# Kernel optimization log

Hardware: AMD Instinct MI355X
Metric: run time of the kernel (lower is better)

The kernel has to match this reference:

```python
import jax, jax.numpy as jnp
import numpy as np

BN_EPS = 1e-5


def _square_distance(a, b):
    # a: [B,N,3], b: [B,S,3] -> [B,N,S] squared euclidean distances
    a2 = jnp.sum(a * a, axis=-1)  # [B,N]
    b2 = jnp.sum(b * b, axis=-1)  # [B,S]
    ab = jnp.einsum('bnc,bsc->bns', a, b)
    return a2[:, :, None] + b2[:, None, :] - 2.0 * ab


def _bn_relu(x, gamma, beta, relu=True):
    # x: [B,C,N]; training-mode BatchNorm1d over (B,N)
    mean = jnp.mean(x, axis=(0, 2), keepdims=True)
    var = jnp.var(x, axis=(0, 2), keepdims=True)
    y = (x - mean) * jax.lax.rsqrt(var + BN_EPS)
    y = y * gamma[None, :, None] + beta[None, :, None]
    return jax.nn.relu(y) if relu else y


def _conv1x1(x, w, b):
    # x: [B,C,N], w: [O,C], b: [O]
    return jnp.einsum('oc,bcn->bon', w, x) + b[None, :, None]


def setup_inputs() -> dict:
    key = jax.random.key(0)
    ks = jax.random.split(key, 20)
    B, N, S = 4, 8192, 2048
    D1, D2, C_IN, C_OUT = 128, 256, 384, 256
    s = lambda fan: 1.0 / np.sqrt(fan)
    return {
        'xyz1': jax.random.normal(ks[0], (B, N, 3), jnp.float32),
        'xyz2': jax.random.normal(ks[1], (B, S, 3), jnp.float32),
        'points1': jax.random.normal(ks[2], (B, D1, N), jnp.float32),
        'points2': jax.random.normal(ks[3], (B, D2, S), jnp.float32),
        'fuse_w': jax.random.normal(ks[4], (C_OUT, C_IN), jnp.float32) * s(C_IN),
        'fuse_b': jax.random.normal(ks[5], (C_OUT,), jnp.float32) * s(C_IN),
        'fuse_g': jnp.ones((C_OUT,), jnp.float32),
        'fuse_be': jnp.zeros((C_OUT,), jnp.float32),
        'e1_w': jax.random.normal(ks[6], (C_OUT, C_OUT), jnp.float32) * s(C_OUT),
        'e1_b': jax.random.normal(ks[7], (C_OUT,), jnp.float32) * s(C_OUT),
        'e1_g': jnp.ones((C_OUT,), jnp.float32),
        'e1_be': jnp.zeros((C_OUT,), jnp.float32),
        'e2_w': jax.random.normal(ks[8], (C_OUT, C_OUT), jnp.float32) * s(C_OUT),
        'e2_b': jax.random.normal(ks[9], (C_OUT,), jnp.float32) * s(C_OUT),
        'e2_g': jnp.ones((C_OUT,), jnp.float32),
        'e2_be': jnp.zeros((C_OUT,), jnp.float32),
        'k': 3,
    }


def reference(xyz1, xyz2, points1, points2, fuse_w, fuse_b, fuse_g, fuse_be,
              e1_w, e1_b, e1_g, e1_be, e2_w, e2_b, e2_g, e2_be, k):
    B, N, _ = xyz1.shape
    p2 = jnp.transpose(points2, (0, 2, 1))  # [B,S,D2]

    # --- KNN (k smallest squared distances), equivalent to sort[:, :, :k] ---
    dists = _square_distance(xyz1, xyz2)             # [B,N,S]
    neg_d, idx = jax.lax.top_k(-dists, k)            # ascending distances
    d = -neg_d                                       # [B,N,k]

    # --- inverse-distance weighted interpolation ---
    recip = 1.0 / (d + 1e-8)
    weight = recip / jnp.sum(recip, axis=2, keepdims=True)  # [B,N,k]
    gathered = jax.vmap(lambda p, i: p[i])(p2, idx)          # [B,N,k,D2]
    interp = jnp.sum(gathered * weight[..., None], axis=2)   # [B,N,D2]

    # --- concat skip features, fuse, extraction ---
    p1 = jnp.transpose(points1, (0, 2, 1))           # [B,N,D1]
    new_pts = jnp.concatenate([p1, interp], axis=-1) # [B,N,D1+D2]
    x = jnp.transpose(new_pts, (0, 2, 1))            # [B,C_in,N]

    x = _bn_relu(_conv1x1(x, fuse_w, fuse_b), fuse_g, fuse_be)      # fuse
    y = _bn_relu(_conv1x1(x, e1_w, e1_b), e1_g, e1_be)              # net1
    y = _bn_relu(_conv1x1(y, e2_w, e2_b), e2_g, e2_be, relu=False)  # net2
    return jax.nn.relu(y + x)                                       # residual
```

## Files before the change

### kernel.cpp

```cpp
#include <hip/hip_runtime.h>

#define NPTS 8192
#define SPTS 2048
#define BATCH 4
#define CO 256
#define TOTAL_ROWS (BATCH * NPTS)

typedef __attribute__((ext_vector_type(4))) float f32x4;
typedef __attribute__((ext_vector_type(8))) short bf16x8s;
typedef __attribute__((ext_vector_type(4))) unsigned short u16x4;
typedef __attribute__((ext_vector_type(8))) unsigned short u16x8;
typedef __attribute__((ext_vector_type(4))) unsigned int u32x4;

__device__ __forceinline__ unsigned short f2bf(float f) {
  unsigned int u = __float_as_uint(f);
  u += 0x7FFFu + ((u >> 16) & 1u);
  return (unsigned short)(u >> 16);
}
__device__ __forceinline__ float bf2f(unsigned short h) {
  return __uint_as_float(((unsigned int)h) << 16);
}
__device__ __forceinline__ unsigned int cvtpk(float lo, float hi) {
  unsigned int r;
  asm("v_cvt_pk_bf16_f32 %0, %1, %2" : "=v"(r) : "v"(lo), "v"(hi));
  return r;
}
__device__ __forceinline__ void gload_lds16(const void* g, void* l) {
  __builtin_amdgcn_global_load_lds((const __attribute__((address_space(1))) void*)g,
                                   (__attribute__((address_space(3))) void*)l, 16, 0, 0);
}


__device__ __forceinline__ void transpose_body(
    const float* __restrict__ in, unsigned short* __restrict__ out,
    int C, int S, int KT, int packed, int bx, int by, int bz, int t,
    float (*LT)[65]) {
  const int s0 = bx * 64, c0 = by * 64;
  const float* inb = in + (size_t)bz * C * S;
  const int cr = t >> 4, sq = t & 15;
  #pragma unroll
  for (int it = 0; it < 4; ++it) {
    int cc = cr + it * 16;
    float4 v = *reinterpret_cast<const float4*>(inb + (size_t)(c0 + cc) * S + s0 + sq * 4);
    LT[sq * 4 + 0][cc] = v.x; LT[sq * 4 + 1][cc] = v.y;
    LT[sq * 4 + 2][cc] = v.z; LT[sq * 4 + 3][cc] = v.w;
  }
  __syncthreads();
  const int sr = t >> 2, cq = t & 3;
  u16x8 o0v, o1v;
  #pragma unroll
  for (int k = 0; k < 8; ++k) o0v[k] = f2bf(LT[sr][cq * 16 + k]);
  #pragma unroll
  for (int k = 0; k < 8; ++k) o1v[k] = f2bf(LT[sr][cq * 16 + 8 + k]);
  if (packed) {
    size_t rg = (size_t)bz * S + s0 + sr;
    int c = c0 + cq * 16;
    size_t ad = ((rg >> 4) * KT + (c >> 5)) * 512 + ((c >> 3) & 3) * 128 + (rg & 15) * 8;
    *reinterpret_cast<u16x8*>(out + ad) = o0v;
    *reinterpret_cast<u16x8*>(out + ad + 128) = o1v;
  } else {
    unsigned short* op = out + ((size_t)bz * S + s0 + sr) * 256 + c0 + cq * 16;
    *reinterpret_cast<u16x8*>(op) = o0v;
    *reinterpret_cast<u16x8*>(op + 8) = o1v;
  }
}

__global__ __launch_bounds__(256) void prep_all(
    const float* __restrict__ points2, unsigned short* __restrict__ p2t,
    const float* __restrict__ points1, unsigned short* __restrict__ X1,
    const float* __restrict__ w1, const float* __restrict__ w2,
    const float* __restrict__ w3, unsigned short* __restrict__ o1,
    unsigned short* __restrict__ o2, unsigned short* __restrict__ o3,
    const float* __restrict__ xyz2, float4* __restrict__ sptg) {
  __shared__ float LT[64][65];
  const int bid = blockIdx.x, t = threadIdx.x;
  if (bid < 512) {
    int x = bid & 31, y = (bid >> 5) & 3, z = bid >> 7;
    transpose_body(points2, p2t, 256, SPTS, 0, 0, x, y, z, t, LT);
  } else if (bid < 1536) {
    int b2 = bid - 512;
    int x = b2 & 127, y = (b2 >> 7) & 1, z = b2 >> 8;
    transpose_body(points1, X1, 128, NPTS, 12, 1, x, y, z, t, LT);
  } else if (bid < 1648) {
    int gid = (bid - 1536) * 256 + t;
    const float* src;
    unsigned short* dst;
    int K, cl;
    if (gid < 12288) { src = w1; dst = o1; K = 384; cl = gid; }
    else if (gid < 20480) { src = w2; dst = o2; K = 256; cl = gid - 12288; }
    else if (gid < 28672) { src = w3; dst = o3; K = 256; cl = gid - 20480; }
    else return;
    int cpo = K >> 3;
    int o = cl / cpo, k0 = (cl - o * cpo) * 8;
    float4 a = *reinterpret_cast<const float4*>(src + (size_t)o * K + k0);
    float4 b = *reinterpret_cast<const float4*>(src + (size_t)o * K + k0 + 4);
    u16x8 v;
    v[0] = f2bf(a.x); v[1] = f2bf(a.y); v[2] = f2bf(a.z); v[3] = f2bf(a.w);
    v[4] = f2bf(b.x); v[5] = f2bf(b.y); v[6] = f2bf(b.z); v[7] = f2bf(b.w);
    int KT = K >> 5;
    size_t ad = ((size_t)(o >> 4) * KT + (k0 >> 5)) * 512 + ((k0 >> 3) & 3) * 128 + (o & 15) * 8;
    *reinterpret_cast<u16x8*>(dst + ad) = v;
  } else {
    int gid = (bid - 1648) * 256 + t;
    const float* p = xyz2 + (size_t)gid * 3;
    float x = p[0], y = p[1], z = p[2];
    float b2 = __fadd_rn(__fadd_rn(__fmul_rn(x, x), __fmul_rn(y, y)), __fmul_rn(z, z));
    sptg[gid] = make_float4(x, y, z, b2);
  }
}

#define CSINS(q, dd, s)                                                    \
  do {                                                                     \
    float tt = dd; int ti = s;                                             \
    bool c0 = tt < d0[q];                                                  \
    float h = c0 ? d0[q] : tt; int hi_ = c0 ? i0[q] : ti;                  \
    d0[q] = c0 ? tt : d0[q];   i0[q] = c0 ? ti : i0[q];                    \
    tt = h; ti = hi_;                                                      \
    bool c1 = tt < d1[q];                                                  \
    h = c1 ? d1[q] : tt; hi_ = c1 ? i1[q] : ti;                            \
    d1[q] = c1 ? tt : d1[q];   i1[q] = c1 ? ti : i1[q];                    \
    tt = h; ti = hi_;                                                      \
    bool c2 = tt < d2[q];                                                  \
    d2[q] = c2 ? tt : d2[q];   i2[q] = c2 ? ti : i2[q];                    \
  } while (0)

#define INSK(x)                                                            \
  do {                                                                     \
    bool c0 = (x) < k0, c1 = (x) < k1, c2 = (x) < k2;                      \
    unsigned long long nk0 = c0 ? (x) : k0;                                \
    unsigned long long nk1 = c0 ? k0 : (c1 ? (x) : k1);                    \
    unsigned long long nk2 = c1 ? k1 : (c2 ? (x) : k2);                    \
    k0 = nk0; k1 = nk1; k2 = nk2;                                          \
  } while (0)

__device__ __forceinline__ unsigned long long packdi(float d, int i) {
  unsigned int b = __float_as_uint(d);
  unsigned int u = b ^ ((unsigned int)((int)b >> 31) | 0x80000000u);
  return ((unsigned long long)u << 32) | (unsigned int)i;
}
__device__ __forceinline__ float unpackd(unsigned long long k) {
  unsigned int u = (unsigned int)(k >> 32);
  unsigned int b = u ^ ((u & 0x80000000u) ? 0x80000000u : 0xFFFFFFFFu);
  return __uint_as_float(b);
}

__global__ __launch_bounds__(256) void knn_gather(
    const float* __restrict__ xyz1, const float4* __restrict__ sptg,
    const unsigned short* __restrict__ p2t, unsigned short* __restrict__ X1) {
  const int b = blockIdx.y, t = threadIdx.x;
  const int wave = t >> 6, lane = t & 63;
  const int nb = blockIdx.x * 16 + wave * 4;
  const float4* sp = sptg + (size_t)b * SPTS;

  float qx[4], qy[4], qz[4], a2[4];
  float d0[4], d1[4], d2[4];
  int i0[4], i1[4], i2[4];
  #pragma unroll
  for (int q = 0; q < 4; ++q) {
    const float* qp = xyz1 + ((size_t)b * NPTS + nb + q) * 3;
    qx[q] = qp[0]; qy[q] = qp[1]; qz[q] = qp[2];
    a2[q] = __fadd_rn(__fadd_rn(__fmul_rn(qx[q], qx[q]), __fmul_rn(qy[q], qy[q])),
                      __fmul_rn(qz[q], qz[q]));
    d0[q] = 1e30f; d1[q] = 1e30f; d2[q] = 1e30f;
    i0[q] = 0; i1[q] = 0; i2[q] = 0;
  }

  #pragma unroll 2
  for (int it = 0; it < SPTS / 128; ++it) {
    int sA = it * 128 + lane;
    int sB = sA + 64;
    float4 pA = sp[sA];
    float4 pB = sp[sB];
    #pragma unroll
    for (int q = 0; q < 4; ++q) {
      float dotA = __fadd_rn(__fadd_rn(__fmul_rn(qx[q], pA.x), __fmul_rn(qy[q], pA.y)),
                             __fmul_rn(qz[q], pA.z));
      float dA = __fsub_rn(__fadd_rn(a2[q], pA.w), __fmul_rn(2.0f, dotA));
      float dotB = __fadd_rn(__fadd_rn(__fmul_rn(qx[q], pB.x), __fmul_rn(qy[q], pB.y)),
                             __fmul_rn(qz[q], pB.z));
      float dB = __fsub_rn(__fadd_rn(a2[q], pB.w), __fmul_rn(2.0f, dotB));
      CSINS(q, dA, sA);
      CSINS(q, dB, sB);
    }
  }

  #pragma unroll
  for (int q = 0; q < 4; ++q) {
    unsigned long long k0 = packdi(d0[q], i0[q]);
    unsigned long long k1 = packdi(d1[q], i1[q]);
    unsigned long long k2 = packdi(d2[q], i2[q]);
    #pragma unroll
    for (int m = 1; m < 64; m <<= 1) {
      unsigned long long x0 = __shfl_xor(k0, m);
      unsigned long long x1 = __shfl_xor(k1, m);
      unsigned long long x2 = __shfl_xor(k2, m);
      INSK(x0); INSK(x1); INSK(x2);
    }
    int j0 = (int)(k0 & 0xFFFFFFFFu);
    int j1 = (int)(k1 & 0xFFFFFFFFu);
    int j2 = (int)(k2 & 0xFFFFFFFFu);
    float r0 = 1.0f / __fadd_rn(unpackd(k0), 1e-8f);
    float r1 = 1.0f / __fadd_rn(unpackd(k1), 1e-8f);
    float r2 = 1.0f / __fadd_rn(unpackd(k2), 1e-8f);
    float rs = __fadd_rn(__fadd_rn(r0, r1), r2);
    float w0 = r0 / rs, w1 = r1 / rs, w2 = r2 / rs;

    const unsigned short* rw0 = p2t + ((size_t)b * SPTS + j0) * 256 + lane * 4;
    const unsigned short* rw1 = p2t + ((size_t)b * SPTS + j1) * 256 + lane * 4;
    const unsigned short* rw2 = p2t + ((size_t)b * SPTS + j2) * 256 + lane * 4;
    u16x4 v0 = *reinterpret_cast<const u16x4*>(rw0);
    u16x4 v1 = *reinterpret_cast<const u16x4*>(rw1);
    u16x4 v2 = *reinterpret_cast<const u16x4*>(rw2);
    u16x4 o;
    #pragma unroll
    for (int e = 0; e < 4; ++e) {
      float f = w0 * bf2f(v0[e]) + w1 * bf2f(v1[e]) + w2 * bf2f(v2[e]);
      o[e] = f2bf(f);
    }
    size_t rg = (size_t)b * NPTS + nb + q;
    int ca = 128 + lane * 4;
    size_t ad = (rg >> 4) * 12 * 512 + (rg & 15) * 8 + (size_t)(ca >> 5) * 512 +
                ((ca >> 3) & 3) * 128 + (ca & 7);
    *reinterpret_cast<u16x4*>(X1 + ad) = o;
  }
}

template <int K, bool BNIN>
__global__ __launch_bounds__(256) void gemm_packed(
    const unsigned short* __restrict__ Wp, const unsigned short* __restrict__ Xp,
    const float* __restrict__ ssp, const float* __restrict__ bias,
    unsigned short* __restrict__ Z, float* __restrict__ part) {
  constexpr int KT = K / 32;
  __shared__ unsigned short Ws[4 * KT * 512];
  const int t = threadIdx.x, wave = t >> 6, lane = t & 63;
  const int lr = lane & 15, hi4 = lane >> 4;
  const int id = blockIdx.x;
  const int wg = (id & 7) * 64 + (id >> 3);
  const int br = wg >> 2;
  const int cb = wg & 3;

  const unsigned short* Xb = Xp + ((size_t)(br * 16 + wave * 4) * KT) * 512 + lane * 8;
  u16x8 xp[3][4];
  #pragma unroll
  for (int d = 0; d < 3; ++d)
    #pragma unroll
    for (int rr = 0; rr < 4; ++rr)
      xp[d][rr] = *reinterpret_cast<const u16x8*>(Xb + ((size_t)rr * KT + d) * 512);

  const unsigned short* Wsrc = Wp + (size_t)cb * 4 * KT * 512;
  constexpr int WCH = 4 * KT * 512 / 8;
  #pragma unroll
  for (int i = 0; i < WCH / 256; ++i)
    gload_lds16(Wsrc + (size_t)(t + i * 256) * 8, Ws + (t + i * 256) * 8);
  __syncthreads();

  f32x4 acc[4][4];
  #pragma unroll
  for (int rr = 0; rr < 4; ++rr)
    #pragma unroll
    for (int ot = 0; ot < 4; ++ot) acc[rr][ot] = (f32x4)0.f;

  #pragma unroll
  for (int kt = 0; kt < KT; ++kt) {
    const int slot = kt % 3;
    u16x8 xc[4];
    #pragma unroll
    for (int rr = 0; rr < 4; ++rr) xc[rr] = xp[slot][rr];
    if (kt + 3 < KT) {
      #pragma unroll
      for (int rr = 0; rr < 4; ++rr)
        xp[slot][rr] = *reinterpret_cast<const u16x8*>(Xb + ((size_t)rr * KT + kt + 3) * 512);
    }
    bf16x8s xf[4];
    if constexpr (BNIN) {
      const int cbase = kt * 32 + hi4 * 8;
      f32x4 s0 = *reinterpret_cast<const f32x4*>(ssp + cbase);
      f32x4 s1 = *reinterpret_cast<const f32x4*>(ssp + cbase + 4);
      f32x4 h0 = *reinterpret_cast<const f32x4*>(ssp + 256 + cbase);
      f32x4 h1 = *reinterpret_cast<const f32x4*>(ssp + 256 + cbase + 4);
      #pragma unroll
      for (int rr = 0; rr < 4; ++rr) {
        float y0 = fmaxf(s0[0] * bf2f(xc[rr][0]) + h0[0], 0.f);
        float y1 = fmaxf(s0[1] * bf2f(xc[rr][1]) + h0[1], 0.f);
        float y2 = fmaxf(s0[2] * bf2f(xc[rr][2]) + h0[2], 0.f);
        float y3 = fmaxf(s0[3] * bf2f(xc[rr][3]) + h0[3], 0.f);
        float y4 = fmaxf(s1[0] * bf2f(xc[rr][4]) + h1[0], 0.f);
        float y5 = fmaxf(s1[1] * bf2f(xc[rr][5]) + h1[1], 0.f);
        float y6 = fmaxf(s1[2] * bf2f(xc[rr][6]) + h1[2], 0.f);
        float y7 = fmaxf(s1[3] * bf2f(xc[rr][7]) + h1[3], 0.f);
        u32x4 xw = {cvtpk(y0, y1), cvtpk(y2, y3), cvtpk(y4, y5), cvtpk(y6, y7)};
        xf[rr] = *reinterpret_cast<bf16x8s*>(&xw);
      }
    } else {
      #pragma unroll
      for (int rr = 0; rr < 4; ++rr)
        xf[rr] = *reinterpret_cast<bf16x8s*>(&xc[rr]);
    }
    bf16x8s wf[4];
    #pragma unroll
    for (int ot = 0; ot < 4; ++ot)
      wf[ot] = *reinterpret_cast<const bf16x8s*>(Ws + (size_t)(ot * KT + kt) * 512 + lane * 8);
    #pragma unroll
    for (int rr = 0; rr < 4; ++rr)
      #pragma unroll
      for (int ot = 0; ot < 4; ++ot)
        acc[rr][ot] =
            __builtin_amdgcn_mfma_f32_16x16x32_bf16(wf[ot], xf[rr], acc[rr][ot], 0, 0, 0);
  }

  const size_t pbase = (size_t)(br * 4 + wave) * 512;
  #pragma unroll
  for (int ot = 0; ot < 4; ++ot) {
    const int o_c = cb * 64 + ot * 16 + hi4 * 4;
    f32x4 bv = *reinterpret_cast<const f32x4*>(bias + o_c);
    const int kto = o_c >> 5, hb = (o_c >> 3) & 3, e0 = o_c & 7;
    float sm[4] = {0.f, 0.f, 0.f, 0.f}, sq[4] = {0.f, 0.f, 0.f, 0.f};
    #pragma unroll
    for (int rr = 0; rr < 4; ++rr) {
      f32x4 v = acc[rr][ot] + bv;
      #pragma unroll
      for (int e = 0; e < 4; ++e) {
        sm[e] += v[e];
        sq[e] += v[e] * v[e];
      }
      unsigned int o01 = cvtpk(v[0], v[1]);
      unsigned int o23 = cvtpk(v[2], v[3]);
      size_t rtg = (size_t)br * 16 + wave * 4 + rr;
      size_t ad = (rtg * 8 + kto) * 512 + hb * 128 + lr * 8 + e0;
      *reinterpret_cast<uint2*>(Z + ad) = make_uint2(o01, o23);
    }
    #pragma unroll
    for (int m = 8; m >= 1; m >>= 1) {
      #pragma unroll
      for (int e = 0; e < 4; ++e) {
        sm[e] += __shfl_xor(sm[e], m);
        sq[e] += __shfl_xor(sq[e], m);
      }
    }
    if (lr == 0) {
      f32x4 vs = {sm[0], sm[1], sm[2], sm[3]};
      f32x4 vq = {sq[0], sq[1], sq[2], sq[3]};
      *reinterpret_cast<f32x4*>(part + pbase + o_c) = vs;
      *reinterpret_cast<f32x4*>(part + pbase + 256 + o_c) = vq;
    }
  }
}

__global__ __launch_bounds__(256) void reduce_stats(
    const float* __restrict__ part, const float* __restrict__ gamma,
    const float* __restrict__ beta, float* __restrict__ ss) {
  __shared__ float red[32][8];
  const int t = threadIdx.x;
  const int sg = t >> 3, co = t & 7;
  const int c = (co < 4) ? (blockIdx.x * 4 + co) : (256 + blockIdx.x * 4 + (co - 4));
  float sm = 0.f;
  #pragma unroll
  for (int k = 0; k < 16; ++k)
    sm += part[(size_t)(sg + 32 * k) * 512 + c];
  red[sg][co] = sm;
  __syncthreads();
  if (t < 8) {
    float s = 0.f;
    #pragma unroll
    for (int g = 0; g < 32; ++g) s += red[g][t];
    red[0][t] = s;
  }
  __syncthreads();
  if (t < 4) {
    int ch = blockIdx.x * 4 + t;
    const float inv = 1.0f / (float)TOTAL_ROWS;
    float mean = red[0][t] * inv;
    float var = red[0][t + 4] * inv - mean * mean;
    float sc = gamma[ch] * rsqrtf(var + 1e-5f);
    ss[ch] = sc;
    ss[256 + ch] = beta[ch] - mean * sc;
  }
}

__global__ __launch_bounds__(256) void bn_res_out(
    const unsigned short* __restrict__ Z, const unsigned short* __restrict__ Zres,
    const float* __restrict__ ss_res, const float* __restrict__ ss_out,
    float* __restrict__ out) {
  __shared__ float LT[64][65];
  const int b = blockIdx.z, n0 = blockIdx.x * 64, o0 = blockIdx.y * 64;
  const int t = threadIdx.x;
  #pragma unroll
  for (int i = 0; i < 2; ++i) {
    int cid = t + i * 256;
    int r = cid & 15, hi = (cid >> 4) & 3, ktl = (cid >> 6) & 1, rtl = cid >> 7;
    size_t rt = (size_t)b * (NPTS / 16) + (n0 >> 4) + rtl;
    int kt = (o0 >> 5) + ktl;
    size_t ad = (rt * 8 + kt) * 512 + hi * 128 + r * 8;
    u16x8 z = *reinterpret_cast<const u16x8*>(Z + ad);
    u16x8 x = *reinterpret_cast<const u16x8*>(Zres + ad);
    int ob = o0 + ktl * 32 + hi * 8;
    #pragma unroll
    for (int e = 0; e < 8; ++e) {
      int c = ob + e;
      float xv = fmaxf(ss_res[c] * bf2f(x[e]) + ss_res[256 + c], 0.f);
      LT[ktl * 32 + hi * 8 + e][rtl * 16 + r] =
          fmaxf(ss_out[c] * bf2f(z[e]) + ss_out[256 + c] + xv, 0.f);
    }
  }
  __syncthreads();
  const int orow = t >> 2, nq = t & 3;
  float* op = out + ((size_t)b * CO + o0 + orow) * NPTS + n0 + nq * 16;
  #pragma unroll
  for (int j = 0; j < 4; ++j) {
    float4 v = make_float4(LT[orow][nq * 16 + j * 4 + 0], LT[orow][nq * 16 + j * 4 + 1],
                           LT[orow][nq * 16 + j * 4 + 2], LT[orow][nq * 16 + j * 4 + 3]);
    *reinterpret_cast<float4*>(op + j * 4) = v;
  }
}

extern "C" void kernel_launch(void* const* d_in, const int* in_sizes, int n_in,
                              void* d_out, int out_size, void* d_ws, size_t ws_size,
                              hipStream_t stream) {
  const float* xyz1    = (const float*)d_in[0];
  const float* xyz2    = (const float*)d_in[1];
  const float* points1 = (const float*)d_in[2];
  const float* points2 = (const float*)d_in[3];
  const float* fuse_w  = (const float*)d_in[4];
  const float* fuse_b  = (const float*)d_in[5];
  const float* fuse_g  = (const float*)d_in[6];
  const float* fuse_be = (const float*)d_in[7];
  const float* e1_w    = (const float*)d_in[8];
  const float* e1_b    = (const float*)d_in[9];
  const float* e1_g    = (const float*)d_in[10];
  const float* e1_be   = (const float*)d_in[11];
  const float* e2_w    = (const float*)d_in[12];
  const float* e2_b    = (const float*)d_in[13];
  const float* e2_g    = (const float*)d_in[14];
  const float* e2_be   = (const float*)d_in[15];
  float* out = (float*)d_out;

  char* w = (char*)d_ws;
  auto carve = [&](size_t bytes) {
    char* p = w;
    w += (bytes + 255) & ~(size_t)255;
    return p;
  };
  unsigned short* Wb1 = (unsigned short*)carve(98304 * 2);
  unsigned short* Wb2 = (unsigned short*)carve(65536 * 2);
  unsigned short* Wb3 = (unsigned short*)carve(65536 * 2);
  unsigned short* p2t = (unsigned short*)carve((size_t)BATCH * SPTS * 256 * 2);
  float4* sptg        = (float4*)carve((size_t)BATCH * SPTS * 16);
  unsigned short* X1  = (unsigned short*)carve((size_t)TOTAL_ROWS * 384 * 2);
  unsigned short* Z1  = (unsigned short*)carve((size_t)TOTAL_ROWS * 256 * 2);
  unsigned short* Z2  = (unsigned short*)carve((size_t)TOTAL_ROWS * 256 * 2);
  unsigned short* Z3  = (unsigned short*)carve((size_t)TOTAL_ROWS * 256 * 2);
  float* part         = (float*)carve((size_t)512 * 512 * 4);
  float* ss           = (float*)carve(3 * 512 * 4);

  prep_all<<<dim3(1680), 256, 0, stream>>>(points2, p2t, points1, X1,
                                           fuse_w, e1_w, e2_w, Wb1, Wb2, Wb3,
                                           xyz2, sptg);

  knn_gather<<<dim3(NPTS / 16, BATCH), 256, 0, stream>>>(xyz1, sptg, p2t, X1);

  gemm_packed<384, false><<<dim3(512), 256, 0, stream>>>(Wb1, X1, nullptr, fuse_b, Z1, part);
  reduce_stats<<<dim3(64), 256, 0, stream>>>(part, fuse_g, fuse_be, ss);

  gemm_packed<256, true><<<dim3(512), 256, 0, stream>>>(Wb2, Z1, ss, e1_b, Z2, part);
  reduce_stats<<<dim3(64), 256, 0, stream>>>(part, e1_g, e1_be, ss + 512);

  gemm_packed<256, true><<<dim3(512), 256, 0, stream>>>(Wb3, Z2, ss + 512, e2_b, Z3, part);
  reduce_stats<<<dim3(64), 256, 0, stream>>>(part, e2_g, e2_be, ss + 1024);

  bn_res_out<<<dim3(NPTS / 64, 4, BATCH), 256, 0, stream>>>(Z3, Z1, ss, ss + 1024, out);
}
```

Before: 145.1 us.

## Fuse three GEMM+BatchNorm stages into one cooperative persistent kernel

Replaces the three GEMM launches, three stat-reduction launches and the final residual kernel with a single cooperative kernel of 512 blocks that uses grid.sync between stages. Each block keeps its GEMM accumulators in registers across the grid barrier, reduces the BN statistics itself, and writes only the normalized bf16 activations. This avoids writing and re-reading pre-BN intermediates and removes per-launch overhead. It relies on all 512 blocks being co-resident (two per CU under launch bounds), and if the cooperative launch fails it falls back to the old multi-kernel path.

```diff
diff --git a/kernel.cpp b/kernel.cpp
--- a/kernel.cpp
+++ b/kernel.cpp
@@ -1,10 +1,13 @@
 #include <hip/hip_runtime.h>
+#include <hip/hip_cooperative_groups.h>
 
 #define NPTS 8192
 #define SPTS 2048
 #define BATCH 4
 #define CO 256
 #define TOTAL_ROWS (BATCH * NPTS)
+
+namespace cg = cooperative_groups;
 
 typedef __attribute__((ext_vector_type(4))) float f32x4;
 typedef __attribute__((ext_vector_type(8))) short bf16x8s;
@@ -413,6 +416,232 @@
   }
 }
 
+template <int K>
+__device__ __forceinline__ void mega_gemm(
+    const unsigned short* __restrict__ Wp, const unsigned short* __restrict__ Xp,
+    const float* __restrict__ bias, float* __restrict__ part,
+    unsigned short* Ws, f32x4 (&acc)[4][4],
+    int t, int wave, int lane, int lr, int hi4, int br, int cb) {
+  constexpr int KT = K / 32;
+  const unsigned short* Xb = Xp + ((size_t)(br * 16 + wave * 4) * KT) * 512 + lane * 8;
+  u16x8 xpf[3][4];
+  #pragma unroll
+  for (int d = 0; d < 3; ++d)
+    #pragma unroll
+    for (int rr = 0; rr < 4; ++rr)
+      xpf[d][rr] = *reinterpret_cast<const u16x8*>(Xb + ((size_t)rr * KT + d) * 512);
+
+  const unsigned short* Wsrc = Wp + (size_t)cb * 4 * KT * 512;
+  constexpr int WCH = 4 * KT * 512 / 8;
+  #pragma unroll
+  for (int i = 0; i < WCH / 256; ++i)
+    gload_lds16(Wsrc + (size_t)(t + i * 256) * 8, Ws + (t + i * 256) * 8);
+  __syncthreads();
+
+  #pragma unroll
+  for (int rr = 0; rr < 4; ++rr)
+    #pragma unroll
+    for (int ot = 0; ot < 4; ++ot) acc[rr][ot] = (f32x4)0.f;
+
+  #pragma unroll
+  for (int kt = 0; kt < KT; ++kt) {
+    const int slot = kt % 3;
+    u16x8 xc[4];
+    #pragma unroll
+    for (int rr = 0; rr < 4; ++rr) xc[rr] = xpf[slot][rr];
+    if (kt + 3 < KT) {
+      #pragma unroll
+      for (int rr = 0; rr < 4; ++rr)
+        xpf[slot][rr] = *reinterpret_cast<const u16x8*>(Xb + ((size_t)rr * KT + kt + 3) * 512);
+    }
+    bf16x8s wf[4];
+    #pragma unroll
+    for (int ot = 0; ot < 4; ++ot)
+      wf[ot] = *reinterpret_cast<const bf16x8s*>(Ws + (size_t)(ot * KT + kt) * 512 + lane * 8);
+    #pragma unroll
+    for (int rr = 0; rr < 4; ++rr)
+      #pragma unroll
+      for (int ot = 0; ot < 4; ++ot)
+        acc[rr][ot] = __builtin_amdgcn_mfma_f32_16x16x32_bf16(
+            wf[ot], *reinterpret_cast<bf16x8s*>(&xc[rr]), acc[rr][ot], 0, 0, 0);
+  }
+
+  const size_t pbase = (size_t)(br * 4 + wave) * 512;
+  #pragma unroll
+  for (int ot = 0; ot < 4; ++ot) {
+    const int o_c = cb * 64 + ot * 16 + hi4 * 4;
+    f32x4 bv = *reinterpret_cast<const f32x4*>(bias + o_c);
+    float sm[4] = {0.f, 0.f, 0.f, 0.f}, sq[4] = {0.f, 0.f, 0.f, 0.f};
+    #pragma unroll
+    for (int rr = 0; rr < 4; ++rr) {
+      acc[rr][ot] += bv;
+      #pragma unroll
+      for (int e = 0; e < 4; ++e) {
+        sm[e] += acc[rr][ot][e];
+        sq[e] += acc[rr][ot][e] * acc[rr][ot][e];
+      }
+    }
+    #pragma unroll
+    for (int m = 8; m >= 1; m >>= 1) {
+      #pragma unroll
+      for (int e = 0; e < 4; ++e) {
+        sm[e] += __shfl_xor(sm[e], m);
+        sq[e] += __shfl_xor(sq[e], m);
+      }
+    }
+    if (lr == 0) {
+      f32x4 vs = {sm[0], sm[1], sm[2], sm[3]};
+      f32x4 vq = {sq[0], sq[1], sq[2], sq[3]};
+      *reinterpret_cast<f32x4*>(part + pbase + o_c) = vs;
+      *reinterpret_cast<f32x4*>(part + pbase + 256 + o_c) = vq;
+    }
+  }
+}
+
+__device__ __forceinline__ void stats_ss(
+    const float* __restrict__ part, const float* __restrict__ gamma,
+    const float* __restrict__ beta, float* redf, int t, int cb) {
+  const int cl = t & 63, qs = t >> 6;
+  const int c = cb * 64 + cl;
+  float sm = 0.f, sq = 0.f;
+  #pragma unroll 4
+  for (int i = 0; i < 128; ++i) {
+    int s = qs * 128 + i;
+    sm += part[(size_t)s * 512 + c];
+    sq += part[(size_t)s * 512 + 256 + c];
+  }
+  redf[qs * 128 + cl * 2] = sm;
+  redf[qs * 128 + cl * 2 + 1] = sq;
+  __syncthreads();
+  if (t < 64) {
+    float s0 = redf[t * 2] + redf[128 + t * 2] + redf[256 + t * 2] + redf[384 + t * 2];
+    float q0 = redf[t * 2 + 1] + redf[128 + t * 2 + 1] + redf[256 + t * 2 + 1] +
+               redf[384 + t * 2 + 1];
+    const float inv = 1.0f / (float)TOTAL_ROWS;
+    float mean = s0 * inv;
+    float var = q0 * inv - mean * mean;
+    float sc = gamma[cb * 64 + t] * rsqrtf(var + 1e-5f);
+    redf[512 + t * 2] = sc;
+    redf[512 + t * 2 + 1] = beta[cb * 64 + t] - mean * sc;
+  }
+  __syncthreads();
+}
+
+__device__ __forceinline__ void epi_writeX(
+    f32x4 (&acc)[4][4], const float* redf, unsigned short* __restrict__ Xdst,
+    int lr, int hi4, int wave, int br, int cb) {
+  #pragma unroll
+  for (int ot = 0; ot < 4; ++ot) {
+    const int o_c = cb * 64 + ot * 16 + hi4 * 4;
+    const int ol = ot * 16 + hi4 * 4;
+    float sc[4], sh[4];
+    #pragma unroll
+    for (int e = 0; e < 4; ++e) {
+      sc[e] = redf[512 + (ol + e) * 2];
+      sh[e] = redf[512 + (ol + e) * 2 + 1];
+    }
+    const int kto = o_c >> 5, hb = (o_c >> 3) & 3, e0 = o_c & 7;
+    #pragma unroll
+    for (int rr = 0; rr < 4; ++rr) {
+      f32x4 v = acc[rr][ot];
+      float y0 = fmaxf(sc[0] * v[0] + sh[0], 0.f);
+      float y1 = fmaxf(sc[1] * v[1] + sh[1], 0.f);
+      float y2 = fmaxf(sc[2] * v[2] + sh[2], 0.f);
+      float y3 = fmaxf(sc[3] * v[3] + sh[3], 0.f);
+      size_t rtg = (size_t)br * 16 + wave * 4 + rr;
+      size_t ad = (rtg * 8 + kto) * 512 + hb * 128 + lr * 8 + e0;
+      *reinterpret_cast<uint2*>(Xdst + ad) = make_uint2(cvtpk(y0, y1), cvtpk(y2, y3));
+    }
+  }
+}
+
+__global__ __launch_bounds__(256, 2) void mega(
+    const unsigned short* __restrict__ Wb1, const unsigned short* __restrict__ Wb2,
+    const unsigned short* __restrict__ Wb3, const unsigned short* __restrict__ X1,
+    unsigned short* __restrict__ X2, unsigned short* __restrict__ X3,
+    const float* __restrict__ b1, const float* __restrict__ b2,
+    const float* __restrict__ b3, const float* __restrict__ g1,
+    const float* __restrict__ be1, const float* __restrict__ g2,
+    const float* __restrict__ be2, const float* __restrict__ g3,
+    const float* __restrict__ be3, float* __restrict__ part,
+    float* __restrict__ out) {
+  __shared__ __align__(16) char smem[49152];
+  unsigned short* Ws = reinterpret_cast<unsigned short*>(smem);
+  float* redf = reinterpret_cast<float*>(smem);
+  cg::grid_group grid = cg::this_grid();
+
+  const int t = threadIdx.x, wave = t >> 6, lane = t & 63;
+  const int lr = lane & 15, hi4 = lane >> 4;
+  const int id = blockIdx.x;
+  const int wg = (id & 7) * 64 + (id >> 3);
+  const int br = wg >> 2, cb = wg & 3;
+
+  f32x4 acc[4][4];
+
+  mega_gemm<384>(Wb1, X1, b1, part, Ws, acc, t, wave, lane, lr, hi4, br, cb);
+  grid.sync();
+  stats_ss(part, g1, be1, redf, t, cb);
+  epi_writeX(acc, redf, X2, lr, hi4, wave, br, cb);
+  grid.sync();
+
+  mega_gemm<256>(Wb2, X2, b2, part, Ws, acc, t, wave, lane, lr, hi4, br, cb);
+  grid.sync();
+  stats_ss(part, g2, be2, redf, t, cb);
+  epi_writeX(acc, redf, X3, lr, hi4, wave, br, cb);
+  grid.sync();
+
+  mega_gemm<256>(Wb3, X3, b3, part, Ws, acc, t, wave, lane, lr, hi4, br, cb);
+  grid.sync();
+  stats_ss(part, g3, be3, redf, t, cb);
+  #pragma unroll
+  for (int ot = 0; ot < 4; ++ot) {
+    const int ol = ot * 16 + hi4 * 4;
+    const int o_c = cb * 64 + ol;
+    float sc[4], sh[4];
+    #pragma unroll
+    for (int e = 0; e < 4; ++e) {
+      sc[e] = redf[512 + (ol + e) * 2];
+      sh[e] = redf[512 + (ol + e) * 2 + 1];
+    }
+    const int kto = o_c >> 5, hb = (o_c >> 3) & 3, e0 = o_c & 7;
+    #pragma unroll
+    for (int rr = 0; rr < 4; ++rr) {
+      size_t rtg = (size_t)br * 16 + wave * 4 + rr;
+      size_t ad = (rtg * 8 + kto) * 512 + hb * 128 + lr * 8 + e0;
+      u16x4 xr = *reinterpret_cast<const u16x4*>(X2 + ad);
+      #pragma unroll
+      for (int e = 0; e < 4; ++e)
+        acc[rr][ot][e] = fmaxf(sc[e] * acc[rr][ot][e] + sh[e] + bf2f(xr[e]), 0.f);
+    }
+  }
+  __syncthreads();
+  float* LT = redf;
+  const int ob = br >> 5;
+  const int nbase = (br & 31) * 256;
+  #pragma unroll
+  for (int c = 0; c < 2; ++c) {
+    if ((wave >> 1) == c) {
+      #pragma unroll
+      for (int ot = 0; ot < 4; ++ot)
+        #pragma unroll
+        for (int rr = 0; rr < 4; ++rr)
+          #pragma unroll
+          for (int e = 0; e < 4; ++e)
+            LT[(size_t)(ot * 16 + hi4 * 4 + e) * 136 + (wave & 1) * 64 + rr * 16 + lr] =
+                acc[rr][ot][e];
+    }
+    __syncthreads();
+    const int o_l = t >> 5, nq = t & 31;
+    #pragma unroll
+    for (int p = 0; p < 8; ++p) {
+      f32x4 v = *reinterpret_cast<const f32x4*>(LT + (size_t)(p * 8 + o_l) * 136 + nq * 4);
+      *reinterpret_cast<f32x4*>(out + ((size_t)(ob * 256 + cb * 64 + p * 8 + o_l)) * NPTS +
+                                nbase + c * 128 + nq * 4) = v;
+    }
+    __syncthreads();
+  }
+}
+
 extern "C" void kernel_launch(void* const* d_in, const int* in_sizes, int n_in,
                               void* d_out, int out_size, void* d_ws, size_t ws_size,
                               hipStream_t stream) {
@@ -446,9 +675,9 @@
   unsigned short* p2t = (unsigned short*)carve((size_t)BATCH * SPTS * 256 * 2);
   float4* sptg        = (float4*)carve((size_t)BATCH * SPTS * 16);
   unsigned short* X1  = (unsigned short*)carve((size_t)TOTAL_ROWS * 384 * 2);
-  unsigned short* Z1  = (unsigned short*)carve((size_t)TOTAL_ROWS * 256 * 2);
-  unsigned short* Z2  = (unsigned short*)carve((size_t)TOTAL_ROWS * 256 * 2);
-  unsigned short* Z3  = (unsigned short*)carve((size_t)TOTAL_ROWS * 256 * 2);
+  unsigned short* bufA= (unsigned short*)carve((size_t)TOTAL_ROWS * 256 * 2);
+  unsigned short* bufB= (unsigned short*)carve((size_t)TOTAL_ROWS * 256 * 2);
+  unsigned short* bufC= (unsigned short*)carve((size_t)TOTAL_ROWS * 256 * 2);
   float* part         = (float*)carve((size_t)512 * 512 * 4);
   float* ss           = (float*)carve(3 * 512 * 4);
 
@@ -458,14 +687,23 @@
 
   knn_gather<<<dim3(NPTS / 16, BATCH), 256, 0, stream>>>(xyz1, sptg, p2t, X1);
 
-  gemm_packed<384, false><<<dim3(512), 256, 0, stream>>>(Wb1, X1, nullptr, fuse_b, Z1, part);
-  reduce_stats<<<dim3(64), 256, 0, stream>>>(part, fuse_g, fuse_be, ss);
-
-  gemm_packed<256, true><<<dim3(512), 256, 0, stream>>>(Wb2, Z1, ss, e1_b, Z2, part);
-  reduce_stats<<<dim3(64), 256, 0, stream>>>(part, e1_g, e1_be, ss + 512);
-
-  gemm_packed<256, true><<<dim3(512), 256, 0, stream>>>(Wb3, Z2, ss + 512, e2_b, Z3, part);
-  reduce_stats<<<dim3(64), 256, 0, stream>>>(part, e2_g, e2_be, ss + 1024);
-
-  bn_res_out<<<dim3(NPTS / 64, 4, BATCH), 256, 0, stream>>>(Z3, Z1, ss, ss + 1024, out);
-}
+  void* args[] = {
+      (void*)&Wb1, (void*)&Wb2, (void*)&Wb3, (void*)&X1, (void*)&bufA, (void*)&bufB,
+      (void*)&fuse_b, (void*)&e1_b, (void*)&e2_b,
+      (void*)&fuse_g, (void*)&fuse_be, (void*)&e1_g, (void*)&e1_be,
+      (void*)&e2_g, (void*)&e2_be, (void*)&part, (void*)&out};
+  hipError_t err = hipLaunchCooperativeKernel(reinterpret_cast<void*>(mega), dim3(512),
+                                              dim3(256), args, 0, stream);
+  if (err != hipSuccess) {
+    gemm_packed<384, false><<<dim3(512), 256, 0, stream>>>(Wb1, X1, nullptr, fuse_b,
+                                                           bufA, part);
+    reduce_stats<<<dim3(64), 256, 0, stream>>>(part, fuse_g, fuse_be, ss);
+    gemm_packed<256, true><<<dim3(512), 256, 0, stream>>>(Wb2, bufA, ss, e1_b, bufB, part);
+    reduce_stats<<<dim3(64), 256, 0, stream>>>(part, e1_g, e1_be, ss + 512);
+    gemm_packed<256, true><<<dim3(512), 256, 0, stream>>>(Wb3, bufB, ss + 512, e2_b,
+                                                          bufC, part);
+    reduce_stats<<<dim3(64), 256, 0, stream>>>(part, e2_g, e2_be, ss + 1024);
+    bn_res_out<<<dim3(NPTS / 64, 4, BATCH), 256, 0, stream>>>(bufC, bufA, ss, ss + 1024,
+                                                              out);
+  }
+}
```

New measurement: 411.4 us. 184% more time.
